# Kernel tuning notes

Hardware: AMD Instinct MI355X
Metric: run time of the kernel (lower is better)

The kernel has to match this reference:

```python
import jax, jax.numpy as jnp
import numpy as np

B, S, F_ATT, R, A = 1024, 96, 2048, 512, 512  # batch, att_size, att_feat_size, rnn_size, att_hid_size

def setup_inputs() -> dict:
    key = jax.random.key(0)
    ks = jax.random.split(key, 16)
    def lin(k, out_d, in_d):
        s = 1.0 / np.sqrt(in_d)
        kw, kb = jax.random.split(k)
        return (jax.random.uniform(kw, (out_d, in_d), jnp.float32, -s, s),
                jax.random.uniform(kb, (out_d,), jnp.float32, -s, s))
    W_ae, b_ae = lin(ks[0], R, F_ATT)   # att_embed Linear
    W_c,  b_c  = lin(ks[1], A, R)       # ctx2att
    W_s,  b_s  = lin(ks[2], A, R)       # sentinel_embed
    W_h,  b_h  = lin(ks[3], A, R)       # ho_embed
    W_al, b_al = lin(ks[4], 1, A)       # alpha_net
    W_o,  b_o  = lin(ks[5], R, R)       # att2h
    return {
        'h': jax.random.normal(ks[6], (B, R), jnp.float32),
        'sentinel': jax.random.normal(ks[7], (B, R), jnp.float32),
        'att_feats': jax.random.normal(ks[8], (B, S, F_ATT), jnp.float32),
        'W_ae': W_ae, 'b_ae': b_ae, 'W_c': W_c, 'b_c': b_c,
        'W_s': W_s, 'b_s': b_s, 'W_h': W_h, 'b_h': b_h,
        'W_al': W_al, 'b_al': b_al, 'W_o': W_o, 'b_o': b_o,
    }

def reference(h, sentinel, att_feats, W_ae, b_ae, W_c, b_c, W_s, b_s,
              W_h, b_h, W_al, b_al, W_o, b_o):
    # att_embed: Linear(2048->512) + ReLU (dropout = identity in eval)
    att = jax.nn.relu(jnp.einsum('bsf,rf->bsr', att_feats, W_ae) + b_ae)  # [B,S,R]
    att_embd = jnp.einsum('bsr,ar->bsa', att, W_c) + b_c                   # [B,S,A]
    sent_e = sentinel @ W_s.T + b_s                                        # [B,A]
    h_e = h @ W_h.T + b_h                                                  # [B,A]
    # concat sentinel slot in front of attention features
    img_all = jnp.concatenate([sentinel[:, None, :], att], axis=1)         # [B,S+1,R]
    img_all_embed = jnp.concatenate([sent_e[:, None, :], att_embd], axis=1)  # [B,S+1,A]
    hA = jnp.tanh(img_all_embed + h_e[:, None, :])                         # [B,S+1,A]
    logits = jnp.einsum('bsa,a->bs', hA, W_al[0]) + b_al[0]                # [B,S+1]
    alpha = jax.nn.softmax(logits, axis=-1)
    cHat = jnp.einsum('bs,bsr->br', alpha, img_all)                        # [B,R]
    atten_out = cHat + h
    return jnp.tanh(atten_out @ W_o.T + b_o)                               # [B,R]
```

## Files before the change

kernel.cpp:

```cpp
#include <hip/hip_runtime.h>

#define M1 98304
#define RDIM 512
#define FDIM 2048
#define SDIM 96
#define BM 96
#define BK 64

typedef __attribute__((ext_vector_type(8))) __bf16 bf16x8;
typedef __attribute__((ext_vector_type(4))) float f32x4;

#define WAITV6 asm volatile("s_waitcnt vmcnt(6)" ::: "memory")
#define WAITV3 asm volatile("s_waitcnt vmcnt(3)" ::: "memory")
#define WAITV0 asm volatile("s_waitcnt vmcnt(0)" ::: "memory")
#define WAITL0 asm volatile("s_waitcnt lgkmcnt(0)" ::: "memory")
#define SBAR   __builtin_amdgcn_s_barrier()
#define SCHED0 __builtin_amdgcn_sched_barrier(0)

__device__ __forceinline__ float bf2f(unsigned short u){
  union { unsigned int i; float f; } v; v.i = ((unsigned int)u) << 16; return v.f;
}
__device__ __forceinline__ unsigned short f2bf(float f){
  union { float f; unsigned int i; } v; v.f = f;
  unsigned int r = v.i + 0x7FFFu + ((v.i >> 16) & 1u);
  return (unsigned short)(r >> 16);
}
__device__ __forceinline__ unsigned short f2bfn(float f){
  __bf16 b = (__bf16)f;
  return __builtin_bit_cast(unsigned short, b);
}
__device__ __forceinline__ float fast_tanh(float x){
  float e = __expf(2.f * x);
  return 1.f - 2.f / (e + 1.f);
}
__device__ __forceinline__ void gld_lds16(const void* g, void* l){
  __builtin_amdgcn_global_load_lds((const __attribute__((address_space(1))) void*)g,
                                   (__attribute__((address_space(3))) void*)l, 16, 0, 0);
}
__device__ __forceinline__ f32x4 mfma16(bf16x8 a, bf16x8 b, f32x4 c){
  return __builtin_amdgcn_mfma_f32_16x16x32_bf16(a, b, c, 0, 0, 0);
}

__device__ __forceinline__ void cat_store_a(const float* __restrict__ src,
                                            unsigned short* __restrict__ dst, int idx){
  float x = src[idx];
  int r = idx >> 9, c = idx & 511;
  unsigned short hi = f2bf(x);
  unsigned short lo = f2bf(x - bf2f(hi));
  unsigned short* p = dst + (long)r * 1536 + c;
  p[0] = hi; p[512] = lo; p[1024] = hi;
}
__device__ __forceinline__ void cat_store_w(const float* __restrict__ src,
                                            unsigned short* __restrict__ dst, int idx){
  float x = src[idx];
  int r = idx >> 9, c = idx & 511;
  unsigned short hi = f2bf(x);
  unsigned short lo = f2bf(x - bf2f(hi));
  unsigned short* p = dst + (long)r * 1536 + c;
  p[0] = hi; p[512] = hi; p[1024] = lo;
}

__global__ void k_convert(const float* W_ae, const float* W_c, const float* W_s,
                          const float* W_h, const float* W_o,
                          const float* h, const float* sent,
                          unsigned short* W_ae_bf, unsigned short* W_c_bf,
                          unsigned short* W_s_cat, unsigned short* W_h_cat,
                          unsigned short* W_o_cat, unsigned short* h_cat,
                          unsigned short* s_cat){
  const int stride = 1024 * 256;
  int i0 = blockIdx.x * 256 + threadIdx.x;
  switch (blockIdx.y) {
    case 0: for (int i = i0; i < 512*2048; i += stride) W_ae_bf[i] = f2bf(W_ae[i]); break;
    case 1: for (int i = i0; i < 512*512;  i += stride) W_c_bf[i]  = f2bf(W_c[i]);  break;
    case 2: for (int i = i0; i < 512*512;  i += stride) cat_store_w(W_s, W_s_cat, i); break;
    case 3: for (int i = i0; i < 512*512;  i += stride) cat_store_w(W_h, W_h_cat, i); break;
    case 4: for (int i = i0; i < 512*512;  i += stride) cat_store_w(W_o, W_o_cat, i); break;
    case 5: for (int i = i0; i < 1024*512; i += stride) cat_store_a(h, h_cat, i); break;
    case 6: for (int i = i0; i < 1024*512; i += stride) cat_store_a(sent, s_cat, i); break;
  }
}

__global__ __launch_bounds__(512) void k_fused(
    const float* __restrict__ Af, const unsigned short* __restrict__ Wae,
    const float* __restrict__ b_ae,
    const unsigned short* __restrict__ Wcg, const float* __restrict__ b_c,
    const float* __restrict__ h_e, const float* __restrict__ W_al,
    const float* __restrict__ sent_e, const float* __restrict__ sent,
    const float* __restrict__ hvec, unsigned short* __restrict__ atten_cat){
  __shared__ __align__(16) char smem[155648];
  unsigned short* As   = (unsigned short*)smem;
  unsigned short* Bs   = (unsigned short*)(smem + 24576);
  unsigned short* attL = (unsigned short*)smem;
  unsigned short* Wcs  = (unsigned short*)(smem + 98304);
  float* part = (float*)(smem + 131072);
  float* lg   = (float*)(smem + 131072 + 1536);
  float* alp  = (float*)(smem + 131072 + 1536 + 512);
  float* ssum = (float*)(smem + 131072 + 1536 + 1024);

  const int tid = threadIdx.x;
  const int w = tid >> 6, l = tid & 63;
  const int wm = w >> 2, wn = w & 3;
  const int b = blockIdx.x;
  const long m0 = (long)b * BM;
  const int g = l >> 4, r15 = l & 15;
  const int rs = r15 & 7;

  f32x4 acc[3][8];
#pragma unroll
  for (int i = 0; i < 3; ++i)
#pragma unroll
    for (int j = 0; j < 8; ++j) acc[i][j] = f32x4{0.f,0.f,0.f,0.f};

  {
    const int brow_in = l >> 3;
    const int bswz = (l & 7) ^ brow_in;
    const unsigned short* bbase = Wae + (long)(w*64 + brow_in) * FDIM + bswz*8;
    int aswz[3];
    const float* abase[3];
#pragma unroll
    for (int s = 0; s < 3; ++s) {
      int c = tid + s*512;
      int arow = c >> 4, akq = c & 15;
      abase[s] = Af + (m0 + arow)*FDIM + akq*4;
      aswz[s] = arow*BK + ((akq ^ ((arow&7)<<1))<<2);
    }
    const int NT = FDIM / BK;
    float4 d0,d1,d2, e0,e1,e2;
    float4 f0 = {0,0,0,0}, f1 = {0,0,0,0}, f2 = {0,0,0,0};

    {
      float4 c0 = *reinterpret_cast<const float4*>(abase[0]);
      float4 c1 = *reinterpret_cast<const float4*>(abase[1]);
      float4 c2 = *reinterpret_cast<const float4*>(abase[2]);
      SCHED0;
#pragma unroll
      for (int q = 0; q < 8; ++q)
        gld_lds16(bbase + (long)q*8*FDIM, Bs + (w*8+q)*512);
      SCHED0;
      d0 = *reinterpret_cast<const float4*>(abase[0] + BK);
      d1 = *reinterpret_cast<const float4*>(abase[1] + BK);
      d2 = *reinterpret_cast<const float4*>(abase[2] + BK);
      e0 = *reinterpret_cast<const float4*>(abase[0] + 2*BK);
      e1 = *reinterpret_cast<const float4*>(abase[1] + 2*BK);
      e2 = *reinterpret_cast<const float4*>(abase[2] + 2*BK);
      SCHED0;
      ushort4 p0; p0.x=f2bfn(c0.x); p0.y=f2bfn(c0.y); p0.z=f2bfn(c0.z); p0.w=f2bfn(c0.w);
      ushort4 p1; p1.x=f2bfn(c1.x); p1.y=f2bfn(c1.y); p1.z=f2bfn(c1.z); p1.w=f2bfn(c1.w);
      ushort4 p2; p2.x=f2bfn(c2.x); p2.y=f2bfn(c2.y); p2.z=f2bfn(c2.z); p2.w=f2bfn(c2.w);
      *reinterpret_cast<ushort4*>(&As[aswz[0]]) = p0;
      *reinterpret_cast<ushort4*>(&As[aswz[1]]) = p1;
      *reinterpret_cast<ushort4*>(&As[aswz[2]]) = p2;
      WAITV6; WAITL0; SCHED0; SBAR; SCHED0;
    }

    int cb = 0;
    for (int kt = 0; kt < NT; ++kt) {
      const int nb = cb ^ 1;
      if (kt + 1 < NT) {
        const long kof = (long)(kt+1) * BK;
#pragma unroll
        for (int q = 0; q < 8; ++q)
          gld_lds16(bbase + (long)q*8*FDIM + kof, Bs + nb*32768 + (w*8+q)*512);
      }
      SCHED0;
      if (kt + 3 < NT) {
        const long kof = (long)(kt+3) * BK;
        f0 = *reinterpret_cast<const float4*>(abase[0] + kof);
        f1 = *reinterpret_cast<const float4*>(abase[1] + kof);
        f2 = *reinterpret_cast<const float4*>(abase[2] + kof);
      }
      SCHED0;
#pragma unroll
      for (int hh = 0; hh < 2; ++hh) {
        const int ko = ((g + 4*hh) ^ rs) << 3;
        bf16x8 afr[3], bfr[8];
#pragma unroll
        for (int i = 0; i < 3; ++i)
          afr[i] = *reinterpret_cast<const bf16x8*>(&As[cb*6144 + (wm*48 + i*16 + r15)*BK + ko]);
#pragma unroll
        for (int j = 0; j < 8; ++j)
          bfr[j] = *reinterpret_cast<const bf16x8*>(&Bs[cb*32768 + (wn*128 + j*16 + r15)*BK + ko]);
        __builtin_amdgcn_s_setprio(1);
#pragma unroll
        for (int i = 0; i < 3; ++i)
#pragma unroll
          for (int j = 0; j < 8; ++j)
            acc[i][j] = mfma16(afr[i], bfr[j], acc[i][j]);
        __builtin_amdgcn_s_setprio(0);
      }
      if (kt + 1 < NT) {
        ushort4 p0; p0.x=f2bfn(d0.x); p0.y=f2bfn(d0.y); p0.z=f2bfn(d0.z); p0.w=f2bfn(d0.w);
        ushort4 p1; p1.x=f2bfn(d1.x); p1.y=f2bfn(d1.y); p1.z=f2bfn(d1.z); p1.w=f2bfn(d1.w);
        ushort4 p2; p2.x=f2bfn(d2.x); p2.y=f2bfn(d2.y); p2.z=f2bfn(d2.z); p2.w=f2bfn(d2.w);
        *reinterpret_cast<ushort4*>(&As[nb*6144 + aswz[0]]) = p0;
        *reinterpret_cast<ushort4*>(&As[nb*6144 + aswz[1]]) = p1;
        *reinterpret_cast<ushort4*>(&As[nb*6144 + aswz[2]]) = p2;
        d0=e0; d1=e1; d2=e2; e0=f0; e1=f1; e2=f2;
        if (kt + 3 < NT) { WAITV3; } else { WAITV0; }
        WAITL0; SCHED0; SBAR; SCHED0;
        cb = nb;
      }
    }
  }
  __syncthreads();
  {
    float bb[8];
#pragma unroll
    for (int j = 0; j < 8; ++j) bb[j] = b_ae[wn*128 + j*16 + r15];
#pragma unroll
    for (int i = 0; i < 3; ++i)
#pragma unroll
      for (int r = 0; r < 4; ++r) {
        int row = wm*48 + i*16 + g*4 + r;
        int rs8 = row & 7;
#pragma unroll
        for (int j = 0; j < 8; ++j) {
          int col = wn*128 + j*16 + r15;
          float x = acc[i][j][r] + bb[j];
          x = x > 0.f ? x : 0.f;
          attL[row*512 + (((col>>3) ^ rs8)<<3) + (col&7)] = f2bfn(x);
        }
      }
  }
  __syncthreads();

#pragma unroll
  for (int i = 0; i < 3; ++i)
#pragma unroll
    for (int j = 0; j < 8; ++j) acc[i][j] = f32x4{0.f,0.f,0.f,0.f};
  {
    const int crow = l >> 2;
    const int bsl2 = (l & 3) ^ ((l >> 3) & 3);
    const int rs2 = (r15 >> 1) & 3;
    uint4 rr0, rr1, rr2, rr3;
    rr0 = *reinterpret_cast<const uint4*>(Wcg + (long)(w*64 + 0*16 + crow)*RDIM + bsl2*8);
    rr1 = *reinterpret_cast<const uint4*>(Wcg + (long)(w*64 + 1*16 + crow)*RDIM + bsl2*8);
    rr2 = *reinterpret_cast<const uint4*>(Wcg + (long)(w*64 + 2*16 + crow)*RDIM + bsl2*8);
    rr3 = *reinterpret_cast<const uint4*>(Wcg + (long)(w*64 + 3*16 + crow)*RDIM + bsl2*8);
    for (int kt = 0; kt < 16; ++kt) {
      *reinterpret_cast<uint4*>(&Wcs[w*2048 + 0*512 + l*8]) = rr0;
      *reinterpret_cast<uint4*>(&Wcs[w*2048 + 1*512 + l*8]) = rr1;
      *reinterpret_cast<uint4*>(&Wcs[w*2048 + 2*512 + l*8]) = rr2;
      *reinterpret_cast<uint4*>(&Wcs[w*2048 + 3*512 + l*8]) = rr3;
      if (kt < 15) {
        const int k0 = (kt+1)*32;
        rr0 = *reinterpret_cast<const uint4*>(Wcg + (long)(w*64 + 0*16 + crow)*RDIM + k0 + bsl2*8);
        rr1 = *reinterpret_cast<const uint4*>(Wcg + (long)(w*64 + 1*16 + crow)*RDIM + k0 + bsl2*8);
        rr2 = *reinterpret_cast<const uint4*>(Wcg + (long)(w*64 + 2*16 + crow)*RDIM + k0 + bsl2*8);
        rr3 = *reinterpret_cast<const uint4*>(Wcg + (long)(w*64 + 3*16 + crow)*RDIM + k0 + bsl2*8);
      }
      WAITL0; SCHED0; SBAR; SCHED0;
      bf16x8 afr[3], bfr[8];
#pragma unroll
      for (int i = 0; i < 3; ++i) {
        int ra = wm*48 + i*16 + r15;
        int grp = (kt<<2) + g;
        afr[i] = *reinterpret_cast<const bf16x8*>(&attL[ra*512 + ((grp ^ rs)<<3)]);
      }
#pragma unroll
      for (int j = 0; j < 8; ++j)
        bfr[j] = *reinterpret_cast<const bf16x8*>(&Wcs[(wn*128 + j*16 + r15)*32 + ((g ^ rs2)<<3)]);
      __builtin_amdgcn_s_setprio(1);
#pragma unroll
      for (int i = 0; i < 3; ++i)
#pragma unroll
        for (int j = 0; j < 8; ++j)
          acc[i][j] = mfma16(afr[i], bfr[j], acc[i][j]);
      __builtin_amdgcn_s_setprio(0);
      WAITL0; SCHED0; SBAR; SCHED0;
    }
  }
  {
    const float* hrow = h_e + (long)b * RDIM;
    float bb2[8], wa[8], he[8];
#pragma unroll
    for (int j = 0; j < 8; ++j) {
      int n = wn*128 + j*16 + r15;
      bb2[j] = b_c[n]; wa[j] = W_al[n]; he[j] = hrow[n];
    }
#pragma unroll
    for (int i = 0; i < 3; ++i)
#pragma unroll
      for (int r = 0; r < 4; ++r) {
        int lrow = wm*48 + i*16 + g*4 + r;
        float s = 0.f;
#pragma unroll
        for (int j = 0; j < 8; ++j) {
          float x = acc[i][j][r] + bb2[j] + he[j];
          s += fast_tanh(x) * wa[j];
        }
        s += __shfl_xor(s, 1); s += __shfl_xor(s, 2);
        s += __shfl_xor(s, 4); s += __shfl_xor(s, 8);
        if (r15 == 0) part[lrow*4 + wn] = s;
      }
  }
  __syncthreads();
  if (tid < 96)
    lg[1+tid] = part[tid*4+0] + part[tid*4+1] + part[tid*4+2] + part[tid*4+3];
  if (tid < 64) {
    float s = 0.f;
    for (int a = tid; a < 512; a += 64)
      s += fast_tanh(sent_e[(long)b*512 + a] + h_e[(long)b*512 + a]) * W_al[a];
    s += __shfl_xor(s, 1); s += __shfl_xor(s, 2); s += __shfl_xor(s, 4);
    s += __shfl_xor(s, 8); s += __shfl_xor(s, 16); s += __shfl_xor(s, 32);
    if (tid == 0) lg[0] = s;
  }
  __syncthreads();
  if (tid < 64) {
    float m = -1e30f;
    for (int i = tid; i < 97; i += 64) m = fmaxf(m, lg[i]);
#pragma unroll
    for (int k = 1; k < 64; k <<= 1) m = fmaxf(m, __shfl_xor(m, k));
    float ss = 0.f;
    for (int i = tid; i < 97; i += 64) { float e = __expf(lg[i] - m); alp[i] = e; ss += e; }
#pragma unroll
    for (int k = 1; k < 64; k <<= 1) ss += __shfl_xor(ss, k);
    if (tid == 0) ssum[0] = ss;
  }
  __syncthreads();
  if (tid < 97) alp[tid] *= (1.f / ssum[0]);
  __syncthreads();
  {
    const int col = tid;
    const int cg = col >> 3, ch = col & 7;
    float accv = alp[0] * sent[(long)b*512 + col];
#pragma unroll 4
    for (int s = 0; s < SDIM; ++s)
      accv += alp[s+1] * bf2f(attL[s*512 + ((cg ^ (s&7))<<3) + ch]);
    float x = accv + hvec[(long)b*512 + col];
    unsigned short hi = f2bf(x);
    unsigned short lo = f2bf(x - bf2f(hi));
    unsigned short* pp = atten_cat + (long)b*1536 + col;
    pp[0] = hi; pp[512] = lo; pp[1024] = hi;
  }
}

__device__ __forceinline__ void small_gemm_body(
    const unsigned short* __restrict__ Abf, const unsigned short* __restrict__ Wb,
    const float* __restrict__ bias, float* __restrict__ Cout, int do_tanh, int bx,
    unsigned short* As, unsigned short* Bs){
  const int tid = threadIdx.x;
  const int w = tid >> 6, l = tid & 63;
  const int wm = w >> 1, wn = w & 1;
  const int m0 = (bx >> 3) * 64, n0 = (bx & 7) * 64;
  const int K = 1536;
  f32x4 acc[2][2];
#pragma unroll
  for (int i = 0; i < 2; ++i)
#pragma unroll
    for (int j = 0; j < 2; ++j) acc[i][j] = f32x4{0.f,0.f,0.f,0.f};

  const int crow = l >> 2;
  const int bsl = (l & 3) ^ ((l >> 3) & 3);
  const unsigned short* arow_p = Abf + (long)(m0 + w*16 + crow)*K + bsl*8;
  const unsigned short* brow_p = Wb  + (long)(n0 + w*16 + crow)*K + bsl*8;

  gld_lds16(arow_p, As + w*512);
  gld_lds16(brow_p, Bs + w*512);
  __syncthreads();
  int cb = 0;
  for (int kt = 0; kt < 48; ++kt) {
    const int nb = cb ^ 1;
    if (kt + 1 < 48) {
      const int k0 = (kt+1) * 32;
      gld_lds16(arow_p + k0, As + nb*2048 + w*512);
      gld_lds16(brow_p + k0, Bs + nb*2048 + w*512);
    }
    bf16x8 afr[2], bfr[2];
    const int g = l >> 4, r15 = l & 15;
    const int rs2 = (r15 >> 1) & 3;
#pragma unroll
    for (int i = 0; i < 2; ++i)
      afr[i] = *reinterpret_cast<const bf16x8*>(As + cb*2048 + (wm*32 + i*16 + r15)*32 + ((g ^ rs2)*8));
#pragma unroll
    for (int j = 0; j < 2; ++j)
      bfr[j] = *reinterpret_cast<const bf16x8*>(Bs + cb*2048 + (wn*32 + j*16 + r15)*32 + ((g ^ rs2)*8));
#pragma unroll
    for (int i = 0; i < 2; ++i)
#pragma unroll
      for (int j = 0; j < 2; ++j)
        acc[i][j] = mfma16(afr[i], bfr[j], acc[i][j]);
    if (kt + 1 < 48) { __syncthreads(); cb = nb; }
  }
  const int r15 = l & 15, g = l >> 4;
#pragma unroll
  for (int i = 0; i < 2; ++i)
#pragma unroll
    for (int r = 0; r < 4; ++r) {
      int m = m0 + wm*32 + i*16 + g*4 + r;
#pragma unroll
      for (int j = 0; j < 2; ++j) {
        int n = n0 + wn*32 + j*16 + r15;
        float x = acc[i][j][r] + bias[n];
        if (do_tanh) x = fast_tanh(x);
        Cout[(long)m * 512 + n] = x;
      }
    }
}

__global__ __launch_bounds__(256) void k_gemm_small(
    const unsigned short* __restrict__ Abf, const unsigned short* __restrict__ Wb,
    const float* __restrict__ bias, float* __restrict__ Cout, int do_tanh){
  __shared__ __align__(16) unsigned short As[2*64*32];
  __shared__ __align__(16) unsigned short Bs[2*64*32];
  small_gemm_body(Abf, Wb, bias, Cout, do_tanh, blockIdx.x, As, Bs);
}

__global__ __launch_bounds__(256) void k_embed2(
    const unsigned short* __restrict__ h_cat, const unsigned short* __restrict__ W_h_cat,
    const float* __restrict__ b_h, float* __restrict__ h_e,
    const unsigned short* __restrict__ s_cat, const unsigned short* __restrict__ W_s_cat,
    const float* __restrict__ b_s, float* __restrict__ sent_e){
  __shared__ __align__(16) unsigned short As[2*64*32];
  __shared__ __align__(16) unsigned short Bs[2*64*32];
  if (blockIdx.y == 0) small_gemm_body(h_cat, W_h_cat, b_h, h_e, 0, blockIdx.x, As, Bs);
  else                 small_gemm_body(s_cat, W_s_cat, b_s, sent_e, 0, blockIdx.x, As, Bs);
}

extern "C" void kernel_launch(void* const* d_in, const int* in_sizes, int n_in,
                              void* d_out, int out_size, void* d_ws, size_t ws_size,
                              hipStream_t stream){
  (void)in_sizes; (void)n_in; (void)out_size; (void)ws_size;
  const float* h    = (const float*)d_in[0];
  const float* sent = (const float*)d_in[1];
  const float* feats= (const float*)d_in[2];
  const float* W_ae = (const float*)d_in[3];
  const float* b_ae = (const float*)d_in[4];
  const float* W_c  = (const float*)d_in[5];
  const float* b_c  = (const float*)d_in[6];
  const float* W_s  = (const float*)d_in[7];
  const float* b_s  = (const float*)d_in[8];
  const float* W_h  = (const float*)d_in[9];
  const float* b_h  = (const float*)d_in[10];
  const float* W_al = (const float*)d_in[11];
  const float* W_o  = (const float*)d_in[13];
  const float* b_o  = (const float*)d_in[14];
  float* out = (float*)d_out;

  char* p = (char*)d_ws;
  unsigned short* W_ae_bf = (unsigned short*)p; p += (size_t)512*2048*2;
  unsigned short* W_c_bf  = (unsigned short*)p; p += (size_t)512*512*2;
  unsigned short* W_s_cat = (unsigned short*)p; p += (size_t)512*1536*2;
  unsigned short* W_h_cat = (unsigned short*)p; p += (size_t)512*1536*2;
  unsigned short* W_o_cat = (unsigned short*)p; p += (size_t)512*1536*2;
  unsigned short* h_cat   = (unsigned short*)p; p += (size_t)1024*1536*2;
  unsigned short* s_cat   = (unsigned short*)p; p += (size_t)1024*1536*2;
  unsigned short* at_cat  = (unsigned short*)p; p += (size_t)1024*1536*2;
  float* h_e    = (float*)p; p += (size_t)1024*512*4;
  float* sent_e = (float*)p; p += (size_t)1024*512*4;

  k_convert<<<dim3(1024,7), 256, 0, stream>>>(W_ae, W_c, W_s, W_h, W_o, h, sent,
        W_ae_bf, W_c_bf, W_s_cat, W_h_cat, W_o_cat, h_cat, s_cat);
  k_embed2<<<dim3(128,2), 256, 0, stream>>>(h_cat, W_h_cat, b_h, h_e,
                                            s_cat, W_s_cat, b_s, sent_e);
  k_fused<<<1024, 512, 0, stream>>>(feats, W_ae_bf, b_ae, W_c_bf, b_c,
                                    h_e, W_al, sent_e, sent, h, at_cat);
  k_gemm_small<<<128, 256, 0, stream>>>(at_cat, W_o_cat, b_o, out, 1);
}
```

Measured before the change: 418.9 us.

## Double fused kernel block to 1024 threads with 2x8 wave tiling

Moves the fused attention kernel from 512 to 1024 threads per block. The 16 waves are arranged 2x8, so each wave covers 64 output columns instead of 128. Accumulator and fragment register use per wave halves, and the staging loads for A, W_ae and W_c are redistributed across more threads. The aim is more waves to hide memory latency within the single LDS-limited block per CU. The cost is twice as many waves at each barrier, smaller per-thread loads (float2 instead of float4), and less B-fragment reuse per wave.

After: 412.5 us. About the same (-1.5%).

```diff
diff --git a/kernel.cpp b/kernel.cpp
--- a/kernel.cpp
+++ b/kernel.cpp
@@ -80,7 +80,7 @@
   }
 }
 
-__global__ __launch_bounds__(512) void k_fused(
+__global__ __launch_bounds__(1024, 4) void k_fused(
     const float* __restrict__ Af, const unsigned short* __restrict__ Wae,
     const float* __restrict__ b_ae,
     const unsigned short* __restrict__ Wcg, const float* __restrict__ b_c,
@@ -93,63 +93,62 @@
   unsigned short* attL = (unsigned short*)smem;
   unsigned short* Wcs  = (unsigned short*)(smem + 98304);
   float* part = (float*)(smem + 131072);
-  float* lg   = (float*)(smem + 131072 + 1536);
-  float* alp  = (float*)(smem + 131072 + 1536 + 512);
-  float* ssum = (float*)(smem + 131072 + 1536 + 1024);
+  float* lg   = (float*)(smem + 131072 + 3072);
+  float* alp  = (float*)(smem + 131072 + 3072 + 512);
+  float* ssum = (float*)(smem + 131072 + 3072 + 1024);
 
   const int tid = threadIdx.x;
   const int w = tid >> 6, l = tid & 63;
-  const int wm = w >> 2, wn = w & 3;
+  const int wm = w >> 3, wn = w & 7;
   const int b = blockIdx.x;
   const long m0 = (long)b * BM;
   const int g = l >> 4, r15 = l & 15;
   const int rs = r15 & 7;
 
-  f32x4 acc[3][8];
+  f32x4 acc[3][4];
 #pragma unroll
   for (int i = 0; i < 3; ++i)
 #pragma unroll
-    for (int j = 0; j < 8; ++j) acc[i][j] = f32x4{0.f,0.f,0.f,0.f};
+    for (int j = 0; j < 4; ++j) acc[i][j] = f32x4{0.f,0.f,0.f,0.f};
 
   {
-    const int brow_in = l >> 3;
-    const int bswz = (l & 7) ^ brow_in;
-    const unsigned short* bbase = Wae + (long)(w*64 + brow_in) * FDIM + bswz*8;
+    const int bswz = (l & 7) ^ (l >> 3);
+    const unsigned short* bbase = Wae + (long)(w*32 + (l >> 3)) * FDIM + bswz*8;
     int aswz[3];
     const float* abase[3];
 #pragma unroll
     for (int s = 0; s < 3; ++s) {
-      int c = tid + s*512;
-      int arow = c >> 4, akq = c & 15;
-      abase[s] = Af + (m0 + arow)*FDIM + akq*4;
-      aswz[s] = arow*BK + ((akq ^ ((arow&7)<<1))<<2);
+      int c = tid + s*1024;
+      int row = c >> 5, kp = c & 31;
+      abase[s] = Af + (m0 + row)*FDIM + kp*2;
+      aswz[s] = row*BK + (((kp>>1) ^ ((row&7)<<1))<<2) + ((kp&1)<<1);
     }
     const int NT = FDIM / BK;
-    float4 d0,d1,d2, e0,e1,e2;
-    float4 f0 = {0,0,0,0}, f1 = {0,0,0,0}, f2 = {0,0,0,0};
+    float2 d0,d1,d2, e0,e1,e2;
+    float2 f0 = {0,0}, f1 = {0,0}, f2 = {0,0};
 
     {
-      float4 c0 = *reinterpret_cast<const float4*>(abase[0]);
-      float4 c1 = *reinterpret_cast<const float4*>(abase[1]);
-      float4 c2 = *reinterpret_cast<const float4*>(abase[2]);
+      float2 c0 = *reinterpret_cast<const float2*>(abase[0]);
+      float2 c1 = *reinterpret_cast<const float2*>(abase[1]);
+      float2 c2 = *reinterpret_cast<const float2*>(abase[2]);
       SCHED0;
 #pragma unroll
-      for (int q = 0; q < 8; ++q)
-        gld_lds16(bbase + (long)q*8*FDIM, Bs + (w*8+q)*512);
+      for (int q = 0; q < 4; ++q)
+        gld_lds16(bbase + (long)q*8*FDIM, Bs + w*2048 + q*512);
       SCHED0;
-      d0 = *reinterpret_cast<const float4*>(abase[0] + BK);
-      d1 = *reinterpret_cast<const float4*>(abase[1] + BK);
-      d2 = *reinterpret_cast<const float4*>(abase[2] + BK);
-      e0 = *reinterpret_cast<const float4*>(abase[0] + 2*BK);
-      e1 = *reinterpret_cast<const float4*>(abase[1] + 2*BK);
-      e2 = *reinterpret_cast<const float4*>(abase[2] + 2*BK);
+      d0 = *reinterpret_cast<const float2*>(abase[0] + BK);
+      d1 = *reinterpret_cast<const float2*>(abase[1] + BK);
+      d2 = *reinterpret_cast<const float2*>(abase[2] + BK);
+      e0 = *reinterpret_cast<const float2*>(abase[0] + 2*BK);
+      e1 = *reinterpret_cast<const float2*>(abase[1] + 2*BK);
+      e2 = *reinterpret_cast<const float2*>(abase[2] + 2*BK);
       SCHED0;
-      ushort4 p0; p0.x=f2bfn(c0.x); p0.y=f2bfn(c0.y); p0.z=f2bfn(c0.z); p0.w=f2bfn(c0.w);
-      ushort4 p1; p1.x=f2bfn(c1.x); p1.y=f2bfn(c1.y); p1.z=f2bfn(c1.z); p1.w=f2bfn(c1.w);
-      ushort4 p2; p2.x=f2bfn(c2.x); p2.y=f2bfn(c2.y); p2.z=f2bfn(c2.z); p2.w=f2bfn(c2.w);
-      *reinterpret_cast<ushort4*>(&As[aswz[0]]) = p0;
-      *reinterpret_cast<ushort4*>(&As[aswz[1]]) = p1;
-      *reinterpret_cast<ushort4*>(&As[aswz[2]]) = p2;
+      *reinterpret_cast<unsigned int*>(&As[aswz[0]]) =
+          (unsigned int)f2bfn(c0.x) | ((unsigned int)f2bfn(c0.y) << 16);
+      *reinterpret_cast<unsigned int*>(&As[aswz[1]]) =
+          (unsigned int)f2bfn(c1.x) | ((unsigned int)f2bfn(c1.y) << 16);
+      *reinterpret_cast<unsigned int*>(&As[aswz[2]]) =
+          (unsigned int)f2bfn(c2.x) | ((unsigned int)f2bfn(c2.y) << 16);
       WAITV6; WAITL0; SCHED0; SBAR; SCHED0;
     }
 
@@ -159,42 +158,42 @@
       if (kt + 1 < NT) {
         const long kof = (long)(kt+1) * BK;
 #pragma unroll
-        for (int q = 0; q < 8; ++q)
-          gld_lds16(bbase + (long)q*8*FDIM + kof, Bs + nb*32768 + (w*8+q)*512);
+        for (int q = 0; q < 4; ++q)
+          gld_lds16(bbase + (long)q*8*FDIM + kof, Bs + nb*32768 + w*2048 + q*512);
       }
       SCHED0;
       if (kt + 3 < NT) {
         const long kof = (long)(kt+3) * BK;
-        f0 = *reinterpret_cast<const float4*>(abase[0] + kof);
-        f1 = *reinterpret_cast<const float4*>(abase[1] + kof);
-        f2 = *reinterpret_cast<const float4*>(abase[2] + kof);
+        f0 = *reinterpret_cast<const float2*>(abase[0] + kof);
+        f1 = *reinterpret_cast<const float2*>(abase[1] + kof);
+        f2 = *reinterpret_cast<const float2*>(abase[2] + kof);
       }
       SCHED0;
 #pragma unroll
       for (int hh = 0; hh < 2; ++hh) {
         const int ko = ((g + 4*hh) ^ rs) << 3;
-        bf16x8 afr[3], bfr[8];
+        bf16x8 afr[3], bfr[4];
 #pragma unroll
         for (int i = 0; i < 3; ++i)
           afr[i] = *reinterpret_cast<const bf16x8*>(&As[cb*6144 + (wm*48 + i*16 + r15)*BK + ko]);
 #pragma unroll
-        for (int j = 0; j < 8; ++j)
-          bfr[j] = *reinterpret_cast<const bf16x8*>(&Bs[cb*32768 + (wn*128 + j*16 + r15)*BK + ko]);
+        for (int j = 0; j < 4; ++j)
+          bfr[j] = *reinterpret_cast<const bf16x8*>(&Bs[cb*32768 + (wn*64 + j*16 + r15)*BK + ko]);
         __builtin_amdgcn_s_setprio(1);
 #pragma unroll
         for (int i = 0; i < 3; ++i)
 #pragma unroll
-          for (int j = 0; j < 8; ++j)
+          for (int j = 0; j < 4; ++j)
             acc[i][j] = mfma16(afr[i], bfr[j], acc[i][j]);
         __builtin_amdgcn_s_setprio(0);
       }
       if (kt + 1 < NT) {
-        ushort4 p0; p0.x=f2bfn(d0.x); p0.y=f2bfn(d0.y); p0.z=f2bfn(d0.z); p0.w=f2bfn(d0.w);
-        ushort4 p1; p1.x=f2bfn(d1.x); p1.y=f2bfn(d1.y); p1.z=f2bfn(d1.z); p1.w=f2bfn(d1.w);
-        ushort4 p2; p2.x=f2bfn(d2.x); p2.y=f2bfn(d2.y); p2.z=f2bfn(d2.z); p2.w=f2bfn(d2.w);
-        *reinterpret_cast<ushort4*>(&As[nb*6144 + aswz[0]]) = p0;
-        *reinterpret_cast<ushort4*>(&As[nb*6144 + aswz[1]]) = p1;
-        *reinterpret_cast<ushort4*>(&As[nb*6144 + aswz[2]]) = p2;
+        *reinterpret_cast<unsigned int*>(&As[nb*6144 + aswz[0]]) =
+            (unsigned int)f2bfn(d0.x) | ((unsigned int)f2bfn(d0.y) << 16);
+        *reinterpret_cast<unsigned int*>(&As[nb*6144 + aswz[1]]) =
+            (unsigned int)f2bfn(d1.x) | ((unsigned int)f2bfn(d1.y) << 16);
+        *reinterpret_cast<unsigned int*>(&As[nb*6144 + aswz[2]]) =
+            (unsigned int)f2bfn(d2.x) | ((unsigned int)f2bfn(d2.y) << 16);
         d0=e0; d1=e1; d2=e2; e0=f0; e1=f1; e2=f2;
         if (kt + 3 < NT) { WAITV3; } else { WAITV0; }
         WAITL0; SCHED0; SBAR; SCHED0;
@@ -204,9 +203,9 @@
   }
   __syncthreads();
   {
-    float bb[8];
-#pragma unroll
-    for (int j = 0; j < 8; ++j) bb[j] = b_ae[wn*128 + j*16 + r15];
+    float bb[4];
+#pragma unroll
+    for (int j = 0; j < 4; ++j) bb[j] = b_ae[wn*64 + j*16 + r15];
 #pragma unroll
     for (int i = 0; i < 3; ++i)
 #pragma unroll
@@ -214,8 +213,8 @@
         int row = wm*48 + i*16 + g*4 + r;
         int rs8 = row & 7;
 #pragma unroll
-        for (int j = 0; j < 8; ++j) {
-          int col = wn*128 + j*16 + r15;
+        for (int j = 0; j < 4; ++j) {
+          int col = wn*64 + j*16 + r15;
           float x = acc[i][j][r] + bb[j];
           x = x > 0.f ? x : 0.f;
           attL[row*512 + (((col>>3) ^ rs8)<<3) + (col&7)] = f2bfn(x);
@@ -227,30 +226,24 @@
 #pragma unroll
   for (int i = 0; i < 3; ++i)
 #pragma unroll
-    for (int j = 0; j < 8; ++j) acc[i][j] = f32x4{0.f,0.f,0.f,0.f};
+    for (int j = 0; j < 4; ++j) acc[i][j] = f32x4{0.f,0.f,0.f,0.f};
   {
-    const int crow = l >> 2;
+    const int lr = l >> 2;
     const int bsl2 = (l & 3) ^ ((l >> 3) & 3);
     const int rs2 = (r15 >> 1) & 3;
-    uint4 rr0, rr1, rr2, rr3;
-    rr0 = *reinterpret_cast<const uint4*>(Wcg + (long)(w*64 + 0*16 + crow)*RDIM + bsl2*8);
-    rr1 = *reinterpret_cast<const uint4*>(Wcg + (long)(w*64 + 1*16 + crow)*RDIM + bsl2*8);
-    rr2 = *reinterpret_cast<const uint4*>(Wcg + (long)(w*64 + 2*16 + crow)*RDIM + bsl2*8);
-    rr3 = *reinterpret_cast<const uint4*>(Wcg + (long)(w*64 + 3*16 + crow)*RDIM + bsl2*8);
+    uint4 rr0, rr1;
+    rr0 = *reinterpret_cast<const uint4*>(Wcg + (long)(w*32 + 0*16 + lr)*RDIM + bsl2*8);
+    rr1 = *reinterpret_cast<const uint4*>(Wcg + (long)(w*32 + 1*16 + lr)*RDIM + bsl2*8);
     for (int kt = 0; kt < 16; ++kt) {
-      *reinterpret_cast<uint4*>(&Wcs[w*2048 + 0*512 + l*8]) = rr0;
-      *reinterpret_cast<uint4*>(&Wcs[w*2048 + 1*512 + l*8]) = rr1;
-      *reinterpret_cast<uint4*>(&Wcs[w*2048 + 2*512 + l*8]) = rr2;
-      *reinterpret_cast<uint4*>(&Wcs[w*2048 + 3*512 + l*8]) = rr3;
+      *reinterpret_cast<uint4*>(&Wcs[w*1024 + 0*512 + l*8]) = rr0;
+      *reinterpret_cast<uint4*>(&Wcs[w*1024 + 1*512 + l*8]) = rr1;
       if (kt < 15) {
         const int k0 = (kt+1)*32;
-        rr0 = *reinterpret_cast<const uint4*>(Wcg + (long)(w*64 + 0*16 + crow)*RDIM + k0 + bsl2*8);
-        rr1 = *reinterpret_cast<const uint4*>(Wcg + (long)(w*64 + 1*16 + crow)*RDIM + k0 + bsl2*8);
-        rr2 = *reinterpret_cast<const uint4*>(Wcg + (long)(w*64 + 2*16 + crow)*RDIM + k0 + bsl2*8);
-        rr3 = *reinterpret_cast<const uint4*>(Wcg + (long)(w*64 + 3*16 + crow)*RDIM + k0 + bsl2*8);
+        rr0 = *reinterpret_cast<const uint4*>(Wcg + (long)(w*32 + 0*16 + lr)*RDIM + k0 + bsl2*8);
+        rr1 = *reinterpret_cast<const uint4*>(Wcg + (long)(w*32 + 1*16 + lr)*RDIM + k0 + bsl2*8);
       }
       WAITL0; SCHED0; SBAR; SCHED0;
-      bf16x8 afr[3], bfr[8];
+      bf16x8 afr[3], bfr[4];
 #pragma unroll
       for (int i = 0; i < 3; ++i) {
         int ra = wm*48 + i*16 + r15;
@@ -258,13 +251,13 @@
         afr[i] = *reinterpret_cast<const bf16x8*>(&attL[ra*512 + ((grp ^ rs)<<3)]);
       }
 #pragma unroll
-      for (int j = 0; j < 8; ++j)
-        bfr[j] = *reinterpret_cast<const bf16x8*>(&Wcs[(wn*128 + j*16 + r15)*32 + ((g ^ rs2)<<3)]);
+      for (int j = 0; j < 4; ++j)
+        bfr[j] = *reinterpret_cast<const bf16x8*>(&Wcs[(wn*64 + j*16 + r15)*32 + ((g ^ rs2)<<3)]);
       __builtin_amdgcn_s_setprio(1);
 #pragma unroll
       for (int i = 0; i < 3; ++i)
 #pragma unroll
-        for (int j = 0; j < 8; ++j)
+        for (int j = 0; j < 4; ++j)
           acc[i][j] = mfma16(afr[i], bfr[j], acc[i][j]);
       __builtin_amdgcn_s_setprio(0);
       WAITL0; SCHED0; SBAR; SCHED0;
@@ -272,10 +265,10 @@
   }
   {
     const float* hrow = h_e + (long)b * RDIM;
-    float bb2[8], wa[8], he[8];
-#pragma unroll
-    for (int j = 0; j < 8; ++j) {
-      int n = wn*128 + j*16 + r15;
+    float bb2[4], wa[4], he[4];
+#pragma unroll
+    for (int j = 0; j < 4; ++j) {
+      int n = wn*64 + j*16 + r15;
       bb2[j] = b_c[n]; wa[j] = W_al[n]; he[j] = hrow[n];
     }
 #pragma unroll
@@ -285,18 +278,22 @@
         int lrow = wm*48 + i*16 + g*4 + r;
         float s = 0.f;
 #pragma unroll
-        for (int j = 0; j < 8; ++j) {
+        for (int j = 0; j < 4; ++j) {
           float x = acc[i][j][r] + bb2[j] + he[j];
           s += fast_tanh(x) * wa[j];
         }
         s += __shfl_xor(s, 1); s += __shfl_xor(s, 2);
         s += __shfl_xor(s, 4); s += __shfl_xor(s, 8);
-        if (r15 == 0) part[lrow*4 + wn] = s;
-      }
-  }
-  __syncthreads();
-  if (tid < 96)
-    lg[1+tid] = part[tid*4+0] + part[tid*4+1] + part[tid*4+2] + part[tid*4+3];
+        if (r15 == 0) part[lrow*8 + wn] = s;
+      }
+  }
+  __syncthreads();
+  if (tid < 96) {
+    float s = 0.f;
+#pragma unroll
+    for (int q = 0; q < 8; ++q) s += part[tid*8 + q];
+    lg[1+tid] = s;
+  }
   if (tid < 64) {
     float s = 0.f;
     for (int a = tid; a < 512; a += 64)
@@ -320,7 +317,7 @@
   __syncthreads();
   if (tid < 97) alp[tid] *= (1.f / ssum[0]);
   __syncthreads();
-  {
+  if (tid < 512) {
     const int col = tid;
     const int cg = col >> 3, ch = col & 7;
     float accv = alp[0] * sent[(long)b*512 + col];
@@ -453,7 +450,7 @@
         W_ae_bf, W_c_bf, W_s_cat, W_h_cat, W_o_cat, h_cat, s_cat);
   k_embed2<<<dim3(128,2), 256, 0, stream>>>(h_cat, W_h_cat, b_h, h_e,
                                             s_cat, W_s_cat, b_s, sent_e);
-  k_fused<<<1024, 512, 0, stream>>>(feats, W_ae_bf, b_ae, W_c_bf, b_c,
-                                    h_e, W_al, sent_e, sent, h, at_cat);
+  k_fused<<<1024, 1024, 0, stream>>>(feats, W_ae_bf, b_ae, W_c_bf, b_c,
+                                     h_e, W_al, sent_e, sent, h, at_cat);
   k_gemm_small<<<128, 256, 0, stream>>>(at_cat, W_o_cat, b_o, out, 1);
 }
```
